# Performance work log

Hardware: AMD Instinct MI355X
Metric: run time of the kernel (lower is better)

The kernel has to match this reference:

```python
import jax, jax.numpy as jnp
import numpy as np

B, N, DIM, DD = 8, 4096, 512, 512
SCALE = DD ** -0.5


def setup_inputs() -> dict:
    key = jax.random.key(0)
    ks = jax.random.split(key, 8)
    x = jax.random.normal(ks[0], (B, N, DIM), dtype=jnp.float32)
    mask = jnp.ones((B, N), dtype=bool)
    # torch nn.Linear(dim, decode_dim, bias=False): weight [DD, DIM], y = x @ W.T
    Wq = jax.random.normal(ks[1], (DD, DIM), dtype=jnp.float32) * (DIM ** -0.5)
    Wk = jax.random.normal(ks[2], (DD, DIM), dtype=jnp.float32) * (DIM ** -0.5)
    Wv = jax.random.normal(ks[3], (DD, DIM), dtype=jnp.float32) * (DIM ** -0.5)
    Wr = jax.random.normal(ks[4], (DD, DD), dtype=jnp.float32) * (DD ** -0.5)
    w_alpha = jax.random.normal(ks[5], (DD,), dtype=jnp.float32)
    w_beta = jax.random.normal(ks[6], (DD,), dtype=jnp.float32)
    return {"x": x, "Wq": Wq, "Wk": Wk, "Wv": Wv, "Wr": Wr,
            "w_alpha": w_alpha, "w_beta": w_beta, "mask": mask}


def _masked_softmax_n(logits, mask):
    # softmax over axis=1 (N), with -inf where mask is False
    logits = jnp.where(mask[:, :, None], logits, -jnp.inf)
    return jax.nn.softmax(logits, axis=1)


def reference(x, Wq, Wk, Wv, Wr, w_alpha, w_beta, mask):
    q = jnp.einsum('bnf,df->bnd', x, Wq)          # [B,N,DD]
    k = jnp.einsum('bnf,df->bnd', x, Wk)
    v = jnp.einsum('bnf,df->bnd', x, Wv)
    alpha = _masked_softmax_n(q * w_alpha * SCALE, mask)   # [B,N,DD]
    global_query = jnp.einsum('bnd,bnd->bd', q, alpha)     # [B,DD]
    p = global_query[:, None, :] * k                       # [B,N,DD]
    beta = _masked_softmax_n(p * w_beta * SCALE, mask)
    global_key = jnp.einsum('bnd,bnd->bd', p, beta)        # [B,DD]
    kv = global_key[:, None, :] * v                        # [B,N,DD]
    out = jnp.einsum('bnd,ed->bne', kv, Wr) + q
    return out
```

## Files before the change

kernel.cpp:

```cpp
#include <hip/hip_runtime.h>

#define N_    4096
#define DD_   512
#define SCALE_ 0.044194173824159216f

typedef unsigned short u16;
typedef __attribute__((ext_vector_type(8))) short bf16x8;
typedef __attribute__((ext_vector_type(4))) float f32x4;

__device__ __forceinline__ float bf2f(u16 u) {
    union { unsigned i; float f; } c; c.i = ((unsigned)u) << 16; return c.f;
}
__device__ __forceinline__ u16 f2bf(float f) {
    union { float f; unsigned u; } c; c.f = f;
    unsigned r = c.u + 0x7FFFu + ((c.u >> 16) & 1u);
    return (u16)(r >> 16);
}
__device__ __forceinline__ void gl_lds(const u16* g, u16* l) {
    __builtin_amdgcn_global_load_lds(
        (const __attribute__((address_space(1))) void*)g,
        (__attribute__((address_space(3))) void*)l, 16, 0, 0);
}

__global__ void cvt_x(const float* __restrict__ s, u16* __restrict__ d)
{
    const size_t i = ((size_t)blockIdx.x * 256 + threadIdx.x) * 8;
    float4 f0 = *(const float4*)(s + i), f1 = *(const float4*)(s + i + 4);
    u16 o[8];
    o[0]=f2bf(f0.x); o[1]=f2bf(f0.y); o[2]=f2bf(f0.z); o[3]=f2bf(f0.w);
    o[4]=f2bf(f1.x); o[5]=f2bf(f1.y); o[6]=f2bf(f1.z); o[7]=f2bf(f1.w);
    *(uint4*)(d + i) = *(uint4*)o;
}

__global__ void cvt_w(const float* s0, const float* s1, u16* d0, u16* d1)
{
    const float* s = blockIdx.z ? s1 : s0;
    u16* d = blockIdx.z ? d1 : d0;
    const size_t i = ((size_t)blockIdx.x * 256 + threadIdx.x) * 8;
    float4 f0 = *(const float4*)(s + i), f1 = *(const float4*)(s + i + 4);
    u16 o[8];
    o[0]=f2bf(f0.x); o[1]=f2bf(f0.y); o[2]=f2bf(f0.z); o[3]=f2bf(f0.w);
    o[4]=f2bf(f1.x); o[5]=f2bf(f1.y); o[6]=f2bf(f1.z); o[7]=f2bf(f1.w);
    *(uint4*)(d + i) = *(uint4*)o;
}

__global__ __launch_bounds__(256)
void gemm_red(const u16* __restrict__ A, const u16* __restrict__ Bt,
              const float* __restrict__ coefV, int mode,
              float* T1, float* T2)
{
    const int g = blockIdx.x;
    const int tileN  = (g >> 3) & 3;
    const int mgroup = (g & 7) | ((g >> 5) << 3);
    const int b = mgroup >> 4;

    __shared__ __align__(16) u16 As[4096], Bs[4096];
    __shared__ float rs1[8][128], rs2[8][128];

    const int tid = threadIdx.x, wave = tid >> 6, lane = tid & 63;
    const int waveM = wave >> 1, waveN = wave & 1;
    const int l15 = lane & 15, quad = lane >> 4;
    const int l4r = lane >> 2, l4c = lane & 3;

    float cf[4];
    #pragma unroll
    for (int ni = 0; ni < 4; ++ni) {
        const int lcol = waveN * 64 + ni * 16 + l15;
        cf[ni] = mode ? coefV[b * 512 + tileN * 128 + lcol]
                      : coefV[tileN * 128 + lcol] * SCALE_;
    }

    const u16* bPtr = Bt + (size_t)(tileN * 128 + wave * 32 + l4r) * 512 + l4c * 8;
    u16* asB = As + wave * 1024;
    u16* bsB = Bs + wave * 1024;

    float s1[4] = {0.f, 0.f, 0.f, 0.f}, s2[4] = {0.f, 0.f, 0.f, 0.f};

    for (int t = 0; t < 2; ++t) {
        const int tileM = mgroup * 2 + t;
        const u16* aPtr = A + (size_t)(tileM * 128 + wave * 32 + l4r) * 512 + l4c * 8;
        f32x4 acc[4][4] = {};

        for (int k0 = 0; k0 < 512; k0 += 32) {
            gl_lds(aPtr + k0, asB); gl_lds(aPtr + k0 + 8192, asB + 512);
            gl_lds(bPtr + k0, bsB); gl_lds(bPtr + k0 + 8192, bsB + 512);
            __syncthreads();
            bf16x8 af[4], bfr[4];
            #pragma unroll
            for (int mi = 0; mi < 4; ++mi)
                af[mi] = *(const bf16x8*)&As[(waveM * 64 + mi * 16 + l15) * 32 + quad * 8];
            #pragma unroll
            for (int ni = 0; ni < 4; ++ni)
                bfr[ni] = *(const bf16x8*)&Bs[(waveN * 64 + ni * 16 + l15) * 32 + quad * 8];
            #pragma unroll
            for (int mi = 0; mi < 4; ++mi)
                #pragma unroll
                for (int ni = 0; ni < 4; ++ni)
                    acc[mi][ni] = __builtin_amdgcn_mfma_f32_16x16x32_bf16(
                        af[mi], bfr[ni], acc[mi][ni], 0, 0, 0);
            __syncthreads();
        }

        #pragma unroll
        for (int ni = 0; ni < 4; ++ni)
            #pragma unroll
            for (int mi = 0; mi < 4; ++mi)
                #pragma unroll
                for (int r = 0; r < 4; ++r) {
                    float v = acc[mi][ni][r];
                    float e = __expf(v * cf[ni]);
                    s1[ni] += e; s2[ni] += v * e;
                }
    }

    const int ridx = waveM * 4 + quad;
    #pragma unroll
    for (int ni = 0; ni < 4; ++ni) {
        const int lcol = waveN * 64 + ni * 16 + l15;
        rs1[ridx][lcol] = s1[ni]; rs2[ridx][lcol] = s2[ni];
    }
    __syncthreads();
    if (tid < 128) {
        float a1 = 0.f, a2 = 0.f;
        #pragma unroll
        for (int j = 0; j < 8; ++j) { a1 += rs1[j][tid]; a2 += rs2[j][tid]; }
        atomicAdd(&T1[b * 512 + tileN * 128 + tid], a1);
        atomicAdd(&T2[b * 512 + tileN * 128 + tid], a2);
    }
}

__global__ void comb1_k(const float* __restrict__ T1, const float* __restrict__ T2,
                        const float* __restrict__ wb, float* gq, float* coefK)
{
    const int i = blockIdx.x * 256 + threadIdx.x;
    const float g = T2[i] / T1[i];
    gq[i] = g;
    coefK[i] = g * wb[i & 511] * SCALE_;
}

__global__ void comb2_k(const float* __restrict__ T1, const float* __restrict__ T2,
                        const float* __restrict__ gq, float* gk)
{
    const int i = blockIdx.x * 256 + threadIdx.x;
    gk[i] = gq[i] * (T2[i] / T1[i]);
}

__global__ void transp_cvt(const float* __restrict__ Wv, u16* WvT)
{
    __shared__ float t[32][33];
    const int f0 = (blockIdx.x & 15) * 32, d0 = (blockIdx.x >> 4) * 32;
    const int c = threadIdx.x & 31, r0 = threadIdx.x >> 5;
    #pragma unroll
    for (int p = 0; p < 4; ++p)
        t[r0 + p * 8][c] = Wv[(size_t)(d0 + r0 + p * 8) * 512 + f0 + c];
    __syncthreads();
    #pragma unroll
    for (int p = 0; p < 4; ++p)
        WvT[(size_t)(f0 + r0 + p * 8) * 512 + d0 + c] = f2bf(t[c][r0 + p * 8]);
}

__global__ void scaleA(const float* __restrict__ Wr, const float* __restrict__ gk, u16* Ap)
{
    const size_t idx0 = ((size_t)blockIdx.x * 256 + threadIdx.x) * 8;
    const int b = (int)(idx0 >> 18);
    const int d = (int)(idx0 & 511);
    const size_t ed = idx0 & ((1u << 18) - 1);
    const float* g = gk + b * 512 + d;
    float4 a0 = *(const float4*)(Wr + ed), a1 = *(const float4*)(Wr + ed + 4);
    u16 o[8];
    o[0]=f2bf(a0.x*g[0]); o[1]=f2bf(a0.y*g[1]); o[2]=f2bf(a0.z*g[2]); o[3]=f2bf(a0.w*g[3]);
    o[4]=f2bf(a1.x*g[4]); o[5]=f2bf(a1.y*g[5]); o[6]=f2bf(a1.z*g[6]); o[7]=f2bf(a1.w*g[7]);
    *(uint4*)(Ap + idx0) = *(uint4*)o;
}

__global__ __launch_bounds__(256)
void gemm_w2(const u16* __restrict__ Ap, const u16* __restrict__ Bt,
             u16* __restrict__ C, const float* __restrict__ addF)
{
    const u16* A = Ap + (size_t)blockIdx.z * 262144;
    u16* Cb = C + (size_t)blockIdx.z * 262144;

    __shared__ __align__(16) u16 As[4096], Bs[4096];
    const int tid = threadIdx.x, wave = tid >> 6, lane = tid & 63;
    const int waveM = wave >> 1, waveN = wave & 1;
    const int l15 = lane & 15, quad = lane >> 4;
    const int l4r = lane >> 2, l4c = lane & 3;
    const int tileN = blockIdx.x, tileM = blockIdx.y;

    f32x4 acc[4][4] = {};
    const u16* aPtr = A  + (size_t)(tileM * 128 + wave * 32 + l4r) * 512 + l4c * 8;
    const u16* bPtr = Bt + (size_t)(tileN * 128 + wave * 32 + l4r) * 512 + l4c * 8;
    u16* asB = As + wave * 1024;
    u16* bsB = Bs + wave * 1024;

    for (int k0 = 0; k0 < 512; k0 += 32) {
        gl_lds(aPtr + k0, asB); gl_lds(aPtr + k0 + 8192, asB + 512);
        gl_lds(bPtr + k0, bsB); gl_lds(bPtr + k0 + 8192, bsB + 512);
        __syncthreads();
        bf16x8 af[4], bfr[4];
        #pragma unroll
        for (int mi = 0; mi < 4; ++mi)
            af[mi] = *(const bf16x8*)&As[(waveM * 64 + mi * 16 + l15) * 32 + quad * 8];
        #pragma unroll
        for (int ni = 0; ni < 4; ++ni)
            bfr[ni] = *(const bf16x8*)&Bs[(waveN * 64 + ni * 16 + l15) * 32 + quad * 8];
        #pragma unroll
        for (int mi = 0; mi < 4; ++mi)
            #pragma unroll
            for (int ni = 0; ni < 4; ++ni)
                acc[mi][ni] = __builtin_amdgcn_mfma_f32_16x16x32_bf16(af[mi], bfr[ni], acc[mi][ni], 0, 0, 0);
        __syncthreads();
    }

    #pragma unroll
    for (int mi = 0; mi < 4; ++mi)
        #pragma unroll
        for (int ni = 0; ni < 4; ++ni) {
            const int row = tileM * 128 + waveM * 64 + mi * 16 + quad * 4;
            const int col = tileN * 128 + waveN * 64 + ni * 16 + l15;
            #pragma unroll
            for (int r = 0; r < 4; ++r) {
                float vv = acc[mi][ni][r] + addF[(size_t)(row + r) * 512 + col];
                Cb[(size_t)(row + r) * 512 + col] = f2bf(vv);
            }
        }
}

__global__ __launch_bounds__(256)
void gemm_out(const u16* __restrict__ A, const u16* __restrict__ W2,
              float* __restrict__ out)
{
    const int g = blockIdx.x;
    const int tileN  = (g >> 3) & 3;
    const int mgroup = (g & 7) | ((g >> 5) << 3);
    const u16* Bt = W2 + (size_t)(mgroup >> 4) * 262144;

    __shared__ __align__(16) u16 As[4096], Bs[4096];
    __shared__ __align__(16) float eb[32 * 132];

    const int tid = threadIdx.x, wave = tid >> 6, lane = tid & 63;
    const int waveM = wave >> 1, waveN = wave & 1;
    const int l15 = lane & 15, quad = lane >> 4;
    const int l4r = lane >> 2, l4c = lane & 3;

    const u16* bPtr = Bt + (size_t)(tileN * 128 + wave * 32 + l4r) * 512 + l4c * 8;
    u16* asB = As + wave * 1024;
    u16* bsB = Bs + wave * 1024;

    for (int t = 0; t < 2; ++t) {
        const int tileM = mgroup * 2 + t;
        const u16* aPtr = A + (size_t)(tileM * 128 + wave * 32 + l4r) * 512 + l4c * 8;
        f32x4 acc[4][4] = {};

        for (int k0 = 0; k0 < 512; k0 += 32) {
            gl_lds(aPtr + k0, asB); gl_lds(aPtr + k0 + 8192, asB + 512);
            gl_lds(bPtr + k0, bsB); gl_lds(bPtr + k0 + 8192, bsB + 512);
            __syncthreads();
            bf16x8 af[4], bfr[4];
            #pragma unroll
            for (int mi = 0; mi < 4; ++mi)
                af[mi] = *(const bf16x8*)&As[(waveM * 64 + mi * 16 + l15) * 32 + quad * 8];
            #pragma unroll
            for (int ni = 0; ni < 4; ++ni)
                bfr[ni] = *(const bf16x8*)&Bs[(waveN * 64 + ni * 16 + l15) * 32 + quad * 8];
            #pragma unroll
            for (int mi = 0; mi < 4; ++mi)
                #pragma unroll
                for (int ni = 0; ni < 4; ++ni)
                    acc[mi][ni] = __builtin_amdgcn_mfma_f32_16x16x32_bf16(
                        af[mi], bfr[ni], acc[mi][ni], 0, 0, 0);
            __syncthreads();
        }

        #pragma unroll
        for (int mi = 0; mi < 4; ++mi) {
            __syncthreads();
            #pragma unroll
            for (int ni = 0; ni < 4; ++ni) {
                const int lrow = waveM * 16 + quad * 4;
                const int lcol = waveN * 64 + ni * 16 + l15;
                #pragma unroll
                for (int r = 0; r < 4; ++r)
                    eb[(lrow + r) * 132 + lcol] = acc[mi][ni][r];
            }
            __syncthreads();
            #pragma unroll
            for (int i = 0; i < 4; ++i) {
                const int f4 = tid + i * 256;
                const int lr = f4 >> 5;
                const int cp = (f4 & 31) * 4;
                const int grow = tileM * 128 + (lr >> 4) * 64 + mi * 16 + (lr & 15);
                float4 vv = *(const float4*)&eb[lr * 132 + cp];
                *(float4*)&out[(size_t)grow * 512 + tileN * 128 + cp] = vv;
            }
        }
    }
}

extern "C" void kernel_launch(void* const* d_in, const int* in_sizes, int n_in,
                              void* d_out, int out_size, void* d_ws, size_t ws_size,
                              hipStream_t stream)
{
    const float* x  = (const float*)d_in[0];
    const float* Wq = (const float*)d_in[1];
    const float* Wk = (const float*)d_in[2];
    const float* Wv = (const float*)d_in[3];
    const float* Wr = (const float*)d_in[4];
    const float* wa = (const float*)d_in[5];
    const float* wb = (const float*)d_in[6];
    float* out = (float*)d_out;

    char* ws = (char*)d_ws;
    float* TQ1   = (float*)(ws);
    float* TQ2   = (float*)(ws + 16 * 1024);
    float* TK1   = (float*)(ws + 32 * 1024);
    float* TK2   = (float*)(ws + 48 * 1024);
    float* gq    = (float*)(ws + 64 * 1024);
    float* coefK = (float*)(ws + 80 * 1024);
    float* gk    = (float*)(ws + 96 * 1024);
    u16*   WvT   = (u16*)  (ws + 112 * 1024);
    u16*   Wqb   = (u16*)  (ws + 624 * 1024);
    u16*   Wkb   = (u16*)  (ws + 1136 * 1024);
    u16*   Ap    = (u16*)  (ws + 1648 * 1024);
    u16*   W2    = (u16*)  (ws + 5744 * 1024);
    u16*   xb    = (u16*)  (ws + 9840 * 1024);

    hipMemsetAsync(TQ1, 0, 64 * 1024, stream);
    cvt_x<<<8192, 256, 0, stream>>>(x, xb);
    cvt_w<<<dim3(128, 1, 2), 256, 0, stream>>>(Wq, Wk, Wqb, Wkb);
    transp_cvt<<<256, 256, 0, stream>>>(Wv, WvT);

    gemm_red<<<512, 256, 0, stream>>>(xb, Wqb, wa, 0, TQ1, TQ2);
    comb1_k<<<16, 256, 0, stream>>>(TQ1, TQ2, wb, gq, coefK);
    gemm_red<<<512, 256, 0, stream>>>(xb, Wkb, coefK, 1, TK1, TK2);
    comb2_k<<<16, 256, 0, stream>>>(TK1, TK2, gq, gk);

    scaleA<<<1024, 256, 0, stream>>>(Wr, gk, Ap);
    gemm_w2<<<dim3(4, 4, 8), 256, 0, stream>>>(Ap, WvT, W2, Wq);

    gemm_out<<<512, 256, 0, stream>>>(xb, W2, out);
}
```

Baseline: 229.3 us.

## Merge Q and K GEMMs into one launch and reduce beta from stored K

Q and K projections now run in a single 1024-block GEMM launch. The K half stores bf16 K into the output buffer instead of waiting for the alpha statistics. A new red2 kernel then computes the beta softmax sums from stored K in chunks, and comb2 combines the partials. This removes the serialized second GEMM pass, at the cost of a 32 MB bf16 write and re-read of K and a strided reduction kernel.

```diff
diff --git a/kernel.cpp b/kernel.cpp
--- a/kernel.cpp
+++ b/kernel.cpp
@@ -45,13 +45,14 @@
 }
 
 __global__ __launch_bounds__(256)
-void gemm_red(const u16* __restrict__ A, const u16* __restrict__ Bt,
-              const float* __restrict__ coefV, int mode,
-              float* T1, float* T2)
+void gemm_qk(const u16* __restrict__ A, const u16* __restrict__ Bq,
+             const u16* __restrict__ Bk, const float* __restrict__ wa,
+             u16* __restrict__ kb, float* T1, float* T2)
 {
     const int g = blockIdx.x;
     const int tileN  = (g >> 3) & 3;
-    const int mgroup = (g & 7) | ((g >> 5) << 3);
+    const int sel    = (g >> 5) & 1;
+    const int mgroup = (g & 7) | ((g >> 6) << 3);
     const int b = mgroup >> 4;
 
     __shared__ __align__(16) u16 As[4096], Bs[4096];
@@ -62,13 +63,12 @@
     const int l15 = lane & 15, quad = lane >> 4;
     const int l4r = lane >> 2, l4c = lane & 3;
 
+    const u16* Bt = sel ? Bk : Bq;
+
     float cf[4];
     #pragma unroll
-    for (int ni = 0; ni < 4; ++ni) {
-        const int lcol = waveN * 64 + ni * 16 + l15;
-        cf[ni] = mode ? coefV[b * 512 + tileN * 128 + lcol]
-                      : coefV[tileN * 128 + lcol] * SCALE_;
-    }
+    for (int ni = 0; ni < 4; ++ni)
+        cf[ni] = wa[tileN * 128 + waveN * 64 + ni * 16 + l15] * SCALE_;
 
     const u16* bPtr = Bt + (size_t)(tileN * 128 + wave * 32 + l4r) * 512 + l4c * 8;
     u16* asB = As + wave * 1024;
@@ -101,31 +101,46 @@
             __syncthreads();
         }
 
-        #pragma unroll
-        for (int ni = 0; ni < 4; ++ni)
-            #pragma unroll
-            for (int mi = 0; mi < 4; ++mi)
-                #pragma unroll
-                for (int r = 0; r < 4; ++r) {
-                    float v = acc[mi][ni][r];
-                    float e = __expf(v * cf[ni]);
-                    s1[ni] += e; s2[ni] += v * e;
+        if (sel) {
+            #pragma unroll
+            for (int mi = 0; mi < 4; ++mi)
+                #pragma unroll
+                for (int ni = 0; ni < 4; ++ni) {
+                    const int row = tileM * 128 + waveM * 64 + mi * 16 + quad * 4;
+                    const int col = tileN * 128 + waveN * 64 + ni * 16 + l15;
+                    #pragma unroll
+                    for (int r = 0; r < 4; ++r)
+                        kb[(size_t)(row + r) * 512 + col] = f2bf(acc[mi][ni][r]);
                 }
-    }
-
-    const int ridx = waveM * 4 + quad;
-    #pragma unroll
-    for (int ni = 0; ni < 4; ++ni) {
-        const int lcol = waveN * 64 + ni * 16 + l15;
-        rs1[ridx][lcol] = s1[ni]; rs2[ridx][lcol] = s2[ni];
-    }
-    __syncthreads();
-    if (tid < 128) {
-        float a1 = 0.f, a2 = 0.f;
-        #pragma unroll
-        for (int j = 0; j < 8; ++j) { a1 += rs1[j][tid]; a2 += rs2[j][tid]; }
-        atomicAdd(&T1[b * 512 + tileN * 128 + tid], a1);
-        atomicAdd(&T2[b * 512 + tileN * 128 + tid], a2);
+        } else {
+            #pragma unroll
+            for (int ni = 0; ni < 4; ++ni)
+                #pragma unroll
+                for (int mi = 0; mi < 4; ++mi)
+                    #pragma unroll
+                    for (int r = 0; r < 4; ++r) {
+                        float v = acc[mi][ni][r];
+                        float e = __expf(v * cf[ni]);
+                        s1[ni] += e; s2[ni] += v * e;
+                    }
+        }
+    }
+
+    if (!sel) {
+        const int ridx = waveM * 4 + quad;
+        #pragma unroll
+        for (int ni = 0; ni < 4; ++ni) {
+            const int lcol = waveN * 64 + ni * 16 + l15;
+            rs1[ridx][lcol] = s1[ni]; rs2[ridx][lcol] = s2[ni];
+        }
+        __syncthreads();
+        if (tid < 128) {
+            float a1 = 0.f, a2 = 0.f;
+            #pragma unroll
+            for (int j = 0; j < 8; ++j) { a1 += rs1[j][tid]; a2 += rs2[j][tid]; }
+            atomicAdd(&T1[b * 512 + tileN * 128 + tid], a1);
+            atomicAdd(&T2[b * 512 + tileN * 128 + tid], a2);
+        }
     }
 }
 
@@ -138,11 +153,34 @@
     coefK[i] = g * wb[i & 511] * SCALE_;
 }
 
-__global__ void comb2_k(const float* __restrict__ T1, const float* __restrict__ T2,
+__global__ void red2(const u16* __restrict__ kb, const float* __restrict__ coefK,
+                     float* P1, float* P2)
+{
+    const int d = blockIdx.x * 256 + threadIdx.x;
+    const int c = blockIdx.y, b = blockIdx.z;
+    const float cfv = coefK[b * 512 + d];
+    const u16* base = kb + ((size_t)(b * N_ + c * 256)) * 512 + d;
+    float s1 = 0.f, s2 = 0.f;
+    for (int i = 0; i < 256; ++i) {
+        float kv = bf2f(base[(size_t)i * 512]);
+        float e  = __expf(kv * cfv);
+        s1 += e; s2 += kv * e;
+    }
+    P1[(b * 16 + c) * 512 + d] = s1;
+    P2[(b * 16 + c) * 512 + d] = s2;
+}
+
+__global__ void comb2_k(const float* __restrict__ P1, const float* __restrict__ P2,
                         const float* __restrict__ gq, float* gk)
 {
     const int i = blockIdx.x * 256 + threadIdx.x;
-    gk[i] = gq[i] * (T2[i] / T1[i]);
+    const int b = i >> 9, d = i & 511;
+    float s1 = 0.f, s2 = 0.f;
+    for (int c = 0; c < 16; ++c) {
+        s1 += P1[(b * 16 + c) * 512 + d];
+        s2 += P2[(b * 16 + c) * 512 + d];
+    }
+    gk[i] = gq[i] * (s2 / s1);
 }
 
 __global__ void transp_cvt(const float* __restrict__ Wv, u16* WvT)
@@ -309,31 +347,32 @@
     const float* wa = (const float*)d_in[5];
     const float* wb = (const float*)d_in[6];
     float* out = (float*)d_out;
+    u16* kb = (u16*)d_out;
 
     char* ws = (char*)d_ws;
     float* TQ1   = (float*)(ws);
     float* TQ2   = (float*)(ws + 16 * 1024);
-    float* TK1   = (float*)(ws + 32 * 1024);
-    float* TK2   = (float*)(ws + 48 * 1024);
-    float* gq    = (float*)(ws + 64 * 1024);
-    float* coefK = (float*)(ws + 80 * 1024);
-    float* gk    = (float*)(ws + 96 * 1024);
-    u16*   WvT   = (u16*)  (ws + 112 * 1024);
-    u16*   Wqb   = (u16*)  (ws + 624 * 1024);
-    u16*   Wkb   = (u16*)  (ws + 1136 * 1024);
-    u16*   Ap    = (u16*)  (ws + 1648 * 1024);
-    u16*   W2    = (u16*)  (ws + 5744 * 1024);
-    u16*   xb    = (u16*)  (ws + 9840 * 1024);
-
-    hipMemsetAsync(TQ1, 0, 64 * 1024, stream);
+    float* gq    = (float*)(ws + 32 * 1024);
+    float* coefK = (float*)(ws + 48 * 1024);
+    float* gk    = (float*)(ws + 64 * 1024);
+    float* P1k   = (float*)(ws + 80 * 1024);
+    float* P2k   = (float*)(ws + 336 * 1024);
+    u16*   WvT   = (u16*)  (ws + 592 * 1024);
+    u16*   Wqb   = (u16*)  (ws + 1104 * 1024);
+    u16*   Wkb   = (u16*)  (ws + 1616 * 1024);
+    u16*   Ap    = (u16*)  (ws + 2128 * 1024);
+    u16*   W2    = (u16*)  (ws + 6224 * 1024);
+    u16*   xb    = (u16*)  (ws + 10320 * 1024);
+
+    hipMemsetAsync(TQ1, 0, 32 * 1024, stream);
     cvt_x<<<8192, 256, 0, stream>>>(x, xb);
     cvt_w<<<dim3(128, 1, 2), 256, 0, stream>>>(Wq, Wk, Wqb, Wkb);
     transp_cvt<<<256, 256, 0, stream>>>(Wv, WvT);
 
-    gemm_red<<<512, 256, 0, stream>>>(xb, Wqb, wa, 0, TQ1, TQ2);
+    gemm_qk<<<1024, 256, 0, stream>>>(xb, Wqb, Wkb, wa, kb, TQ1, TQ2);
     comb1_k<<<16, 256, 0, stream>>>(TQ1, TQ2, wb, gq, coefK);
-    gemm_red<<<512, 256, 0, stream>>>(xb, Wkb, coefK, 1, TK1, TK2);
-    comb2_k<<<16, 256, 0, stream>>>(TK1, TK2, gq, gk);
+    red2<<<dim3(2, 16, 8), 256, 0, stream>>>(kb, coefK, P1k, P2k);
+    comb2_k<<<16, 256, 0, stream>>>(P1k, P2k, gq, gk);
 
     scaleA<<<1024, 256, 0, stream>>>(Wr, gk, Ap);
     gemm_w2<<<dim3(4, 4, 8), 256, 0, stream>>>(Ap, WvT, W2, Wq);
```

Result: slower. 285.6 us (+24.5%).
